# Kernel tuning notes

Measured on AMD Instinct MI355X. Metric: run time of the kernel, lower is better.

## Reference

```python
import jax, jax.numpy as jnp
import numpy as np

D_MODEL = 256
NUM_HEADS = 4
HEAD_DIM = D_MODEL // NUM_HEADS


def setup_inputs() -> dict:
    key = jax.random.key(0)
    ks = jax.random.split(key, 16)
    B, N, M, C = 2, 256, 256, D_MODEL
    inp = {
        'q_tokens': jax.random.normal(ks[0], (B, N, C), jnp.float32),
        'k_tokens': jax.random.normal(ks[1], (B, M, C), jnp.float32),
        'v_tokens': jax.random.normal(ks[2], (B, M, C), jnp.float32),
        'qk_embeds': jax.random.normal(ks[3], (B, N, M, C), jnp.float32),
        'qv_embeds': jax.random.normal(ks[4], (B, N, M, C), jnp.float32),
    }
    scale = 1.0 / np.sqrt(C)
    # Linear layer params (weight used as x @ W + b)
    inp['Wq'] = jax.random.normal(ks[5], (C, C), jnp.float32) * scale
    inp['bq'] = jnp.zeros((C,), jnp.float32)
    inp['Wk'] = jax.random.normal(ks[6], (C, C), jnp.float32) * scale
    inp['bk'] = jnp.zeros((C,), jnp.float32)
    inp['Wv'] = jax.random.normal(ks[7], (C, C), jnp.float32) * scale
    inp['bv'] = jnp.zeros((C,), jnp.float32)
    inp['Wqk'] = jax.random.normal(ks[8], (C, C), jnp.float32) * scale
    inp['bqk'] = jnp.zeros((C,), jnp.float32)
    inp['Wqv'] = jax.random.normal(ks[9], (C, C), jnp.float32) * scale
    inp['bqv'] = jnp.zeros((C,), jnp.float32)
    return inp


def reference(q_tokens, k_tokens, v_tokens, qk_embeds, qv_embeds,
              Wq, bq, Wk, bk, Wv, bv, Wqk, bqk, Wqv, bqv):
    B, N, C = q_tokens.shape
    M = k_tokens.shape[1]
    H, hc = NUM_HEADS, HEAD_DIM

    # token projections -> (B, H, len, hc)
    q = (q_tokens @ Wq + bq).reshape(B, N, H, hc).transpose(0, 2, 1, 3)
    k = (k_tokens @ Wk + bk).reshape(B, M, H, hc).transpose(0, 2, 1, 3)
    v = (v_tokens @ Wv + bv).reshape(B, M, H, hc).transpose(0, 2, 1, 3)

    # pair-embedding projections -> (B, N, M, H, hc)
    qk = (qk_embeds @ Wqk + bqk).reshape(B, N, M, H, hc)
    qv = (qv_embeds @ Wqv + bqv).reshape(B, N, M, H, hc)

    # scores: q . (k + qk)  == q.k + q.qk
    scores = jnp.einsum('bhnc,bhmc->bhnm', q, k)
    scores = scores + jnp.einsum('bhnc,bnmhc->bhnm', q, qk)
    scores = scores / np.sqrt(hc).astype(np.float32)

    attn = jax.nn.softmax(scores, axis=-1)  # (B, H, N, M)

    # output: attn @ (v + qv) == attn@v + attn.qv
    hidden = jnp.einsum('bhnm,bhmc->bhnc', attn, v)
    hidden = hidden + jnp.einsum('bhnm,bnmhc->bhnc', attn, qv)
    hidden = hidden.transpose(0, 2, 1, 3).reshape(B, N, C)  # (B, N, C)
    return hidden, attn
```

## Files before the change

### kernel.cpp

```cpp
#include <hip/hip_runtime.h>

#define BB 2
#define NN 256
#define CC 256

__device__ __forceinline__ float dot4acc(float4 e, float4 w, float s) {
    s = fmaf(e.x, w.x, s); s = fmaf(e.y, w.y, s);
    s = fmaf(e.z, w.z, s); s = fmaf(e.w, w.w, s);
    return s;
}

#define GLL(gaddr, laddr)                                                     \
    __builtin_amdgcn_global_load_lds(                                         \
        (const __attribute__((address_space(1))) void*)(gaddr),               \
        (__attribute__((address_space(3))) void*)(laddr), 16, 0, 0)

#define STAGE_TILE(B, SRCBASE, TT)                                            \
    do {                                                                      \
        const float* _g = (SRCBASE) + (size_t)(TT) * 4096;                    \
        GLL(_g + (w * 2) * 256 + l * 4,     (B) + (w * 2) * 256);             \
        GLL(_g + (w * 2 + 1) * 256 + l * 4, (B) + (w * 2 + 1) * 256);         \
    } while (0)

__global__ __launch_bounds__(256) void proj_gemm(
    const float* __restrict__ q_tok, const float* __restrict__ k_tok, const float* __restrict__ v_tok,
    const float* __restrict__ Wq, const float* __restrict__ bq,
    const float* __restrict__ Wk, const float* __restrict__ bk,
    const float* __restrict__ Wv, const float* __restrict__ bv,
    float* __restrict__ out)
{
    const int row0 = blockIdx.x * 64;
    const int col0 = blockIdx.y * 64;
    const int seg  = row0 >> 9;
    const float* A    = seg == 0 ? q_tok : (seg == 1 ? k_tok : v_tok);
    const float* W    = seg == 0 ? Wq    : (seg == 1 ? Wk    : Wv);
    const float* bias = seg == 0 ? bq    : (seg == 1 ? bk    : bv);
    const int ar0 = row0 & 511;

    __shared__ float As[64][17];
    __shared__ float Bs[16][68];
    const int t  = threadIdx.x;
    const int tr = t >> 4, tc = t & 15;
    float acc[4][4] = {};

    const int sr  = t >> 2, sk4 = (t & 3) << 2;
    const int bkr = t >> 4, bj4 = (t & 15) << 2;

    for (int k0 = 0; k0 < 256; k0 += 16) {
        float4 a4 = *reinterpret_cast<const float4*>(&A[(ar0 + sr) * 256 + k0 + sk4]);
        float4 b4 = *reinterpret_cast<const float4*>(&W[(k0 + bkr) * 256 + col0 + bj4]);
        As[sr][sk4 + 0] = a4.x; As[sr][sk4 + 1] = a4.y; As[sr][sk4 + 2] = a4.z; As[sr][sk4 + 3] = a4.w;
        Bs[bkr][bj4 + 0] = b4.x; Bs[bkr][bj4 + 1] = b4.y; Bs[bkr][bj4 + 2] = b4.z; Bs[bkr][bj4 + 3] = b4.w;
        __syncthreads();
        #pragma unroll
        for (int k = 0; k < 16; ++k) {
            float a[4], bbv[4];
            #pragma unroll
            for (int i = 0; i < 4; ++i) a[i] = As[tr * 4 + i][k];
            #pragma unroll
            for (int j = 0; j < 4; ++j) bbv[j] = Bs[k][tc * 4 + j];
            #pragma unroll
            for (int i = 0; i < 4; ++i)
                #pragma unroll
                for (int j = 0; j < 4; ++j)
                    acc[i][j] = fmaf(a[i], bbv[j], acc[i][j]);
        }
        __syncthreads();
    }
    #pragma unroll
    for (int i = 0; i < 4; ++i) {
        const int r = row0 + tr * 4 + i;
        #pragma unroll
        for (int j = 0; j < 4; ++j) {
            const int cj = col0 + tc * 4 + j;
            out[r * 256 + cj] = acc[i][j] + bias[cj];
        }
    }
}

__global__ __launch_bounds__(256) void qw_gemm(
    const float* __restrict__ qp, const float* __restrict__ Wqk, float* __restrict__ qW)
{
    const int h    = blockIdx.z;
    const int row0 = blockIdx.x * 64;
    const int d0   = blockIdx.y * 64;
    __shared__ float As[64][17];
    __shared__ float Bs[16][68];
    const int t  = threadIdx.x;
    const int tr = t >> 4, tc = t & 15;
    float acc[4][4] = {};
    const int sr = t >> 2, sc4 = (t & 3) << 2;

    for (int k0 = 0; k0 < 64; k0 += 16) {
        float4 a4 = *reinterpret_cast<const float4*>(&qp[(row0 + sr) * 256 + h * 64 + k0 + sc4]);
        float4 b4 = *reinterpret_cast<const float4*>(&Wqk[(d0 + sr) * 256 + h * 64 + k0 + sc4]);
        As[sr][sc4 + 0] = a4.x; As[sr][sc4 + 1] = a4.y; As[sr][sc4 + 2] = a4.z; As[sr][sc4 + 3] = a4.w;
        Bs[sc4 + 0][sr] = b4.x; Bs[sc4 + 1][sr] = b4.y; Bs[sc4 + 2][sr] = b4.z; Bs[sc4 + 3][sr] = b4.w;
        __syncthreads();
        #pragma unroll
        for (int k = 0; k < 16; ++k) {
            float a[4], bbv[4];
            #pragma unroll
            for (int i = 0; i < 4; ++i) a[i] = As[tr * 4 + i][k];
            #pragma unroll
            for (int j = 0; j < 4; ++j) bbv[j] = Bs[k][tc * 4 + j];
            #pragma unroll
            for (int i = 0; i < 4; ++i)
                #pragma unroll
                for (int j = 0; j < 4; ++j)
                    acc[i][j] = fmaf(a[i], bbv[j], acc[i][j]);
        }
        __syncthreads();
    }
    #pragma unroll
    for (int i = 0; i < 4; ++i)
        #pragma unroll
        for (int j = 0; j < 4; ++j)
            qW[((row0 + tr * 4 + i) * 4 + h) * 256 + d0 + tc * 4 + j] = acc[i][j];
}

__global__ __launch_bounds__(256) void qk_gemm(
    const float* __restrict__ qkvp, float* __restrict__ Sqk)
{
    const int bh = blockIdx.z;
    const int b  = bh >> 2, h = bh & 3;
    const int n0 = blockIdx.x * 64;
    const int m0 = blockIdx.y * 64;
    __shared__ float As[64][17];
    __shared__ float Bs[16][68];
    const int t  = threadIdx.x;
    const int tr = t >> 4, tc = t & 15;
    float acc[4][4] = {};
    const int sr = t >> 2, sc4 = (t & 3) << 2;

    for (int k0 = 0; k0 < 64; k0 += 16) {
        float4 a4 = *reinterpret_cast<const float4*>(&qkvp[(size_t)(b * 256 + n0 + sr) * 256 + h * 64 + k0 + sc4]);
        float4 b4 = *reinterpret_cast<const float4*>(&qkvp[(size_t)(512 + b * 256 + m0 + sr) * 256 + h * 64 + k0 + sc4]);
        As[sr][sc4 + 0] = a4.x; As[sr][sc4 + 1] = a4.y; As[sr][sc4 + 2] = a4.z; As[sr][sc4 + 3] = a4.w;
        Bs[sc4 + 0][sr] = b4.x; Bs[sc4 + 1][sr] = b4.y; Bs[sc4 + 2][sr] = b4.z; Bs[sc4 + 3][sr] = b4.w;
        __syncthreads();
        #pragma unroll
        for (int k = 0; k < 16; ++k) {
            float a[4], bbv[4];
            #pragma unroll
            for (int i = 0; i < 4; ++i) a[i] = As[tr * 4 + i][k];
            #pragma unroll
            for (int j = 0; j < 4; ++j) bbv[j] = Bs[k][tc * 4 + j];
            #pragma unroll
            for (int i = 0; i < 4; ++i)
                #pragma unroll
                for (int j = 0; j < 4; ++j)
                    acc[i][j] = fmaf(a[i], bbv[j], acc[i][j]);
        }
        __syncthreads();
    }
    #pragma unroll
    for (int i = 0; i < 4; ++i)
        #pragma unroll
        for (int j = 0; j < 4; ++j)
            Sqk[(size_t)((b * 4 + h) * 256 + n0 + tr * 4 + i) * 256 + m0 + tc * 4 + j] = acc[i][j];
}

__global__ __launch_bounds__(512, 4) void mega6(
    const float* __restrict__ qk_emb, const float* __restrict__ qv_emb,
    const float* __restrict__ qkvp, const float* __restrict__ qW,
    const float* __restrict__ Sqk, const float* __restrict__ Wqv,
    const float* __restrict__ bqv,
    float* __restrict__ attn_out, float* __restrict__ hidden)
{
    const int bn = blockIdx.x;
    const int b  = bn >> 8, n = bn & 255;
    const int t  = threadIdx.x;
    const int w  = t >> 6, l = t & 63;

    __shared__ __align__(16) float buf0[4096];
    __shared__ __align__(16) float buf1[4096];
    __shared__ __align__(16) float qWs[1024];
    __shared__ __align__(16) float SqkL[1024];
    __shared__ __align__(16) float Ssc[1024];
    __shared__ __align__(16) float attn_s[1024];
    __shared__ __align__(16) float Ap[4096];
    __shared__ __align__(16) float pr[2][256];
    __shared__ float mxs[8][4], sums[8][4];

    const float* qkb = qk_emb + (size_t)bn * 65536;
    const float* qvb = qv_emb + (size_t)bn * 65536;

    STAGE_TILE(buf0, qkb, 0);
    {
        const int i2 = t * 2;
        *reinterpret_cast<float2*>(&qWs[i2]) =
            *reinterpret_cast<const float2*>(&qW[(size_t)bn * 1024 + i2]);
        const int h = i2 >> 8, m = i2 & 255;
        *reinterpret_cast<float2*>(&SqkL[i2]) =
            *reinterpret_cast<const float2*>(&Sqk[(size_t)((b * 4 + h) * 256 + n) * 256 + m]);
    }
    __syncthreads();

    const int rl  = l >> 5;
    const int sub = l & 31;
    const int lq  = sub & 15;
    const int hp  = sub >> 4;
    const int rloc = w * 2 + rl;
    const int h0 = hp * 2, h1 = hp * 2 + 1;

    float4 qr0[4], qr1[4];
    #pragma unroll
    for (int c = 0; c < 4; ++c) {
        qr0[c] = *reinterpret_cast<const float4*>(&qWs[h0 * 256 + c * 64 + lq * 4]);
        qr1[c] = *reinterpret_cast<const float4*>(&qWs[h1 * 256 + c * 64 + lq * 4]);
    }

    for (int tt = 0; tt < 16; ++tt) {
        float* cur = (tt & 1) ? buf1 : buf0;
        float* nxt = (tt & 1) ? buf0 : buf1;
        if (tt < 15) STAGE_TILE(nxt, qkb, tt + 1);

        const float* er = cur + rloc * 256 + lq * 4;
        const float4 e0 = *reinterpret_cast<const float4*>(er);
        const float4 e1 = *reinterpret_cast<const float4*>(er + 64);
        const float4 e2 = *reinterpret_cast<const float4*>(er + 128);
        const float4 e3 = *reinterpret_cast<const float4*>(er + 192);
        float s0 = 0.f, s1 = 0.f;
        s0 = dot4acc(e0, qr0[0], s0); s0 = dot4acc(e1, qr0[1], s0);
        s0 = dot4acc(e2, qr0[2], s0); s0 = dot4acc(e3, qr0[3], s0);
        s1 = dot4acc(e0, qr1[0], s1); s1 = dot4acc(e1, qr1[1], s1);
        s1 = dot4acc(e2, qr1[2], s1); s1 = dot4acc(e3, qr1[3], s1);
        s0 += __shfl_xor(s0, 1); s1 += __shfl_xor(s1, 1);
        s0 += __shfl_xor(s0, 2); s1 += __shfl_xor(s1, 2);
        s0 += __shfl_xor(s0, 4); s1 += __shfl_xor(s1, 4);
        s0 += __shfl_xor(s0, 8); s1 += __shfl_xor(s1, 8);
        if ((l & 15) == 0) {
            const int m = tt * 16 + rloc;
            Ssc[h0 * 256 + m] = s0;
            Ssc[h1 * 256 + m] = s1;
        }
        __syncthreads();
    }

    STAGE_TILE(buf0, qvb, 0);

    const int li = l & 31;
    {
        float mxw[4], smw[4];
        #pragma unroll
        for (int h = 0; h < 4; ++h) {
            const float sc = (Ssc[h * 256 + w * 32 + li] + SqkL[h * 256 + w * 32 + li]) * 0.125f;
            float mx = sc;
            #pragma unroll
            for (int mask = 16; mask >= 1; mask >>= 1) mx = fmaxf(mx, __shfl_xor(mx, mask));
            const float e = __expf(sc - mx);
            if (l < 32) attn_s[h * 256 + w * 32 + li] = e;
            float sm = e;
            #pragma unroll
            for (int mask = 16; mask >= 1; mask >>= 1) sm += __shfl_xor(sm, mask);
            mxw[h] = mx; smw[h] = sm;
        }
        if (l == 0) {
            #pragma unroll
            for (int h = 0; h < 4; ++h) { mxs[w][h] = mxw[h]; sums[w][h] = smw[h]; }
        }
    }
    __syncthreads();

    {
        float mgv[4], invv[4];
        #pragma unroll
        for (int h = 0; h < 4; ++h) {
            float mg = mxs[0][h];
            #pragma unroll
            for (int ww = 1; ww < 8; ++ww) mg = fmaxf(mg, mxs[ww][h]);
            float sg = 0.f;
            #pragma unroll
            for (int ww = 0; ww < 8; ++ww) sg += sums[ww][h] * __expf(mxs[ww][h] - mg);
            mgv[h] = mg; invv[h] = 1.f / sg;
        }
        const int h2 = t >> 7, j = t & 127;
        float* ao = attn_out + (size_t)((b * 4 + h2) * 256 + n) * 256;
        #pragma unroll
        for (int rep = 0; rep < 2; ++rep) {
            const int jj = j + rep * 128;
            const float s = __expf(mxs[jj >> 5][h2] - mgv[h2]) * invv[h2];
            const float a = attn_s[h2 * 256 + jj] * s;
            attn_s[h2 * 256 + jj] = a;
            ao[jj] = a;
        }
    }
    __syncthreads();

    float4 acc[4];
    #pragma unroll
    for (int hh = 0; hh < 4; ++hh) acc[hh] = make_float4(0.f, 0.f, 0.f, 0.f);

    for (int tt = 0; tt < 16; ++tt) {
        float* cur = (tt & 1) ? buf1 : buf0;
        float* nxt = (tt & 1) ? buf0 : buf1;
        if (tt < 15) STAGE_TILE(nxt, qvb, tt + 1);

        const int m0 = tt * 16 + w * 2;
        const float4 e0 = *reinterpret_cast<const float4*>(&cur[(w * 2) * 256 + l * 4]);
        const float4 e1 = *reinterpret_cast<const float4*>(&cur[(w * 2 + 1) * 256 + l * 4]);
        #pragma unroll
        for (int hh = 0; hh < 4; ++hh) {
            const float a0 = attn_s[hh * 256 + m0];
            const float a1 = attn_s[hh * 256 + m0 + 1];
            acc[hh].x = fmaf(a0, e0.x, acc[hh].x); acc[hh].y = fmaf(a0, e0.y, acc[hh].y);
            acc[hh].z = fmaf(a0, e0.z, acc[hh].z); acc[hh].w = fmaf(a0, e0.w, acc[hh].w);
            acc[hh].x = fmaf(a1, e1.x, acc[hh].x); acc[hh].y = fmaf(a1, e1.y, acc[hh].y);
            acc[hh].z = fmaf(a1, e1.z, acc[hh].z); acc[hh].w = fmaf(a1, e1.w, acc[hh].w);
        }
        __syncthreads();
    }

    if (w < 4) {
        #pragma unroll
        for (int hh = 0; hh < 4; ++hh)
            *reinterpret_cast<float4*>(&Ap[(w * 4 + hh) * 256 + l * 4]) = acc[hh];
    }
    __syncthreads();
    if (w >= 4) {
        #pragma unroll
        for (int hh = 0; hh < 4; ++hh) {
            float4* p = reinterpret_cast<float4*>(&Ap[((w - 4) * 4 + hh) * 256 + l * 4]);
            float4 o = *p;
            o.x += acc[hh].x; o.y += acc[hh].y; o.z += acc[hh].z; o.w += acc[hh].w;
            *p = o;
        }
    }
    __syncthreads();
    #pragma unroll
    for (int i = 0; i < 2; ++i) {
        const int idx = t + i * 512;
        const int hh = idx >> 8, d = idx & 255;
        Ap[hh * 256 + d] = Ap[hh * 256 + d] + Ap[(4 + hh) * 256 + d]
                         + Ap[(8 + hh) * 256 + d] + Ap[(12 + hh) * 256 + d];
    }

    {
        float* stg = buf0;
        const int c = t & 255, half = t >> 8, hc = c >> 6;
        const int fr0 = t >> 6, fc0 = (t & 63) * 4;
        const int fr1 = fr0 + 8;
        const float* vbase = qkvp + (size_t)(1024 + b * 256) * 256;
        float4 ra = *reinterpret_cast<const float4*>(&vbase[(size_t)fr0 * 256 + fc0]);
        float4 rb = *reinterpret_cast<const float4*>(&vbase[(size_t)fr1 * 256 + fc0]);
        float hv = 0.f;
        for (int mt = 0; mt < 16; ++mt) {
            __syncthreads();
            *reinterpret_cast<float4*>(&stg[fr0 * 256 + fc0]) = ra;
            *reinterpret_cast<float4*>(&stg[fr1 * 256 + fc0]) = rb;
            if (mt < 15) {
                ra = *reinterpret_cast<const float4*>(&vbase[(size_t)((mt + 1) * 16 + fr0) * 256 + fc0]);
                rb = *reinterpret_cast<const float4*>(&vbase[(size_t)((mt + 1) * 16 + fr1) * 256 + fc0]);
            } else {
                ra = *reinterpret_cast<const float4*>(&Wqv[(size_t)fr0 * 256 + fc0]);
                rb = *reinterpret_cast<const float4*>(&Wqv[(size_t)fr1 * 256 + fc0]);
            }
            __syncthreads();
            #pragma unroll
            for (int r = 0; r < 8; ++r)
                hv = fmaf(attn_s[hc * 256 + mt * 16 + half * 8 + r], stg[(half * 8 + r) * 256 + c], hv);
        }
        for (int dt = 0; dt < 16; ++dt) {
            __syncthreads();
            *reinterpret_cast<float4*>(&stg[fr0 * 256 + fc0]) = ra;
            *reinterpret_cast<float4*>(&stg[fr1 * 256 + fc0]) = rb;
            if (dt < 15) {
                ra = *reinterpret_cast<const float4*>(&Wqv[(size_t)((dt + 1) * 16 + fr0) * 256 + fc0]);
                rb = *reinterpret_cast<const float4*>(&Wqv[(size_t)((dt + 1) * 16 + fr1) * 256 + fc0]);
            }
            __syncthreads();
            #pragma unroll
            for (int r = 0; r < 8; ++r)
                hv = fmaf(Ap[hc * 256 + dt * 16 + half * 8 + r], stg[(half * 8 + r) * 256 + c], hv);
        }
        pr[half][c] = hv;
    }
    __syncthreads();
    if (t < 256)
        hidden[(size_t)bn * 256 + t] = pr[0][t] + pr[1][t] + bqv[t];
}

extern "C" void kernel_launch(void* const* d_in, const int* in_sizes, int n_in,
                              void* d_out, int out_size, void* d_ws, size_t ws_size,
                              hipStream_t stream) {
    (void)in_sizes; (void)n_in; (void)out_size; (void)ws_size;
    const float* q_tok  = (const float*)d_in[0];
    const float* k_tok  = (const float*)d_in[1];
    const float* v_tok  = (const float*)d_in[2];
    const float* qk_emb = (const float*)d_in[3];
    const float* qv_emb = (const float*)d_in[4];
    const float* Wq  = (const float*)d_in[5];   const float* bq  = (const float*)d_in[6];
    const float* Wk  = (const float*)d_in[7];   const float* bk  = (const float*)d_in[8];
    const float* Wv  = (const float*)d_in[9];   const float* bv  = (const float*)d_in[10];
    const float* Wqk = (const float*)d_in[11];
    const float* Wqv = (const float*)d_in[13];  const float* bqv = (const float*)d_in[14];

    float* ws   = (float*)d_ws;
    float* qkvp = ws;
    float* qW   = ws + 393216;
    float* Sqk  = ws + 917504;

    float* hidden = (float*)d_out;
    float* attn   = (float*)d_out + BB * NN * CC;

    proj_gemm<<<dim3(24, 4),   256, 0, stream>>>(q_tok, k_tok, v_tok, Wq, bq, Wk, bk, Wv, bv, qkvp);
    qw_gemm  <<<dim3(8, 4, 4), 256, 0, stream>>>(qkvp, Wqk, qW);
    qk_gemm  <<<dim3(4, 4, 8), 256, 0, stream>>>(qkvp, Sqk);
    mega6    <<<512,           512, 0, stream>>>(qk_emb, qv_emb, qkvp, qW, Sqk, Wqv, bqv, attn, hidden);
}
```

Before: 93.41 us.

## Split pair-embedding streaming across M-quarters with split-softmax merge and output GEMM

```diff
diff --git a/kernel.cpp b/kernel.cpp
--- a/kernel.cpp
+++ b/kernel.cpp
@@ -15,9 +15,9 @@
         (const __attribute__((address_space(1))) void*)(gaddr),               \
         (__attribute__((address_space(3))) void*)(laddr), 16, 0, 0)
 
-#define STAGE_TILE(B, SRCBASE, TT)                                            \
+#define STAGE8(B, SRC, TT)                                                    \
     do {                                                                      \
-        const float* _g = (SRCBASE) + (size_t)(TT) * 4096;                    \
+        const float* _g = (SRC) + (size_t)(TT) * 2048;                        \
         GLL(_g + (w * 2) * 256 + l * 4,     (B) + (w * 2) * 256);             \
         GLL(_g + (w * 2 + 1) * 256 + l * 4, (B) + (w * 2 + 1) * 256);         \
     } while (0)
@@ -161,48 +161,39 @@
             Sqk[(size_t)((b * 4 + h) * 256 + n0 + tr * 4 + i) * 256 + m0 + tc * 4 + j] = acc[i][j];
 }
 
-__global__ __launch_bounds__(512, 4) void mega6(
+__global__ __launch_bounds__(256, 6) void stream_kernel(
     const float* __restrict__ qk_emb, const float* __restrict__ qv_emb,
-    const float* __restrict__ qkvp, const float* __restrict__ qW,
-    const float* __restrict__ Sqk, const float* __restrict__ Wqv,
-    const float* __restrict__ bqv,
-    float* __restrict__ attn_out, float* __restrict__ hidden)
+    const float* __restrict__ qW, const float* __restrict__ Sqk,
+    float* __restrict__ Sg, float* __restrict__ stats, float* __restrict__ Aq)
 {
     const int bn = blockIdx.x;
+    const int q  = blockIdx.y;
     const int b  = bn >> 8, n = bn & 255;
     const int t  = threadIdx.x;
     const int w  = t >> 6, l = t & 63;
 
-    __shared__ __align__(16) float buf0[4096];
-    __shared__ __align__(16) float buf1[4096];
+    __shared__ __align__(16) float buf0[2048];
+    __shared__ __align__(16) float buf1[2048];
     __shared__ __align__(16) float qWs[1024];
-    __shared__ __align__(16) float SqkL[1024];
-    __shared__ __align__(16) float Ssc[1024];
-    __shared__ __align__(16) float attn_s[1024];
-    __shared__ __align__(16) float Ap[4096];
-    __shared__ __align__(16) float pr[2][256];
-    __shared__ float mxs[8][4], sums[8][4];
-
-    const float* qkb = qk_emb + (size_t)bn * 65536;
-    const float* qvb = qv_emb + (size_t)bn * 65536;
-
-    STAGE_TILE(buf0, qkb, 0);
+    __shared__ __align__(16) float SqkL[256];
+    __shared__ __align__(16) float Ssc[256];
+    __shared__ __align__(16) float attn_e[256];
+
+    const float* qkb = qk_emb + (size_t)bn * 65536 + (size_t)q * 16384;
+    const float* qvb = qv_emb + (size_t)bn * 65536 + (size_t)q * 16384;
+
+    STAGE8(buf0, qkb, 0);
+    *reinterpret_cast<float4*>(&qWs[t * 4]) =
+        *reinterpret_cast<const float4*>(&qW[(size_t)bn * 1024 + t * 4]);
     {
-        const int i2 = t * 2;
-        *reinterpret_cast<float2*>(&qWs[i2]) =
-            *reinterpret_cast<const float2*>(&qW[(size_t)bn * 1024 + i2]);
-        const int h = i2 >> 8, m = i2 & 255;
-        *reinterpret_cast<float2*>(&SqkL[i2]) =
-            *reinterpret_cast<const float2*>(&Sqk[(size_t)((b * 4 + h) * 256 + n) * 256 + m]);
+        const int h = t >> 6, mi = t & 63;
+        SqkL[t] = Sqk[(size_t)((b * 4 + h) * 256 + n) * 256 + q * 64 + mi];
     }
     __syncthreads();
 
-    const int rl  = l >> 5;
-    const int sub = l & 31;
-    const int lq  = sub & 15;
-    const int hp  = sub >> 4;
-    const int rloc = w * 2 + rl;
-    const int h0 = hp * 2, h1 = hp * 2 + 1;
+    const int lq = l & 15, lr = l >> 4;
+    const int rloc = (w >> 1) * 4 + lr;
+    const int h0 = (w & 1) * 2, h1 = h0 + 1;
 
     float4 qr0[4], qr1[4];
     #pragma unroll
@@ -211,10 +202,10 @@
         qr1[c] = *reinterpret_cast<const float4*>(&qWs[h1 * 256 + c * 64 + lq * 4]);
     }
 
-    for (int tt = 0; tt < 16; ++tt) {
+    for (int tt = 0; tt < 8; ++tt) {
         float* cur = (tt & 1) ? buf1 : buf0;
         float* nxt = (tt & 1) ? buf0 : buf1;
-        if (tt < 15) STAGE_TILE(nxt, qkb, tt + 1);
+        if (tt < 7) STAGE8(nxt, qkb, tt + 1);
 
         const float* er = cur + rloc * 256 + lq * 4;
         const float4 e0 = *reinterpret_cast<const float4*>(er);
@@ -230,98 +221,70 @@
         s0 += __shfl_xor(s0, 2); s1 += __shfl_xor(s1, 2);
         s0 += __shfl_xor(s0, 4); s1 += __shfl_xor(s1, 4);
         s0 += __shfl_xor(s0, 8); s1 += __shfl_xor(s1, 8);
-        if ((l & 15) == 0) {
-            const int m = tt * 16 + rloc;
-            Ssc[h0 * 256 + m] = s0;
-            Ssc[h1 * 256 + m] = s1;
-        }
-        __syncthreads();
-    }
-
-    STAGE_TILE(buf0, qvb, 0);
-
-    const int li = l & 31;
+        if (lq == 0) {
+            const int m = tt * 8 + rloc;
+            Ssc[h0 * 64 + m] = s0;
+            Ssc[h1 * 64 + m] = s1;
+        }
+        __syncthreads();
+    }
+
+    STAGE8(buf0, qvb, 0);
+
     {
-        float mxw[4], smw[4];
-        #pragma unroll
-        for (int h = 0; h < 4; ++h) {
-            const float sc = (Ssc[h * 256 + w * 32 + li] + SqkL[h * 256 + w * 32 + li]) * 0.125f;
-            float mx = sc;
-            #pragma unroll
-            for (int mask = 16; mask >= 1; mask >>= 1) mx = fmaxf(mx, __shfl_xor(mx, mask));
-            const float e = __expf(sc - mx);
-            if (l < 32) attn_s[h * 256 + w * 32 + li] = e;
-            float sm = e;
-            #pragma unroll
-            for (int mask = 16; mask >= 1; mask >>= 1) sm += __shfl_xor(sm, mask);
-            mxw[h] = mx; smw[h] = sm;
-        }
+        const float sc = (Ssc[w * 64 + l] + SqkL[w * 64 + l]) * 0.125f;
+        float mx = sc;
+        #pragma unroll
+        for (int mask = 32; mask >= 1; mask >>= 1) mx = fmaxf(mx, __shfl_xor(mx, mask));
+        const float e = __expf(sc - mx);
+        attn_e[w * 64 + l] = e;
+        float sm = e;
+        #pragma unroll
+        for (int mask = 32; mask >= 1; mask >>= 1) sm += __shfl_xor(sm, mask);
+        Sg[(size_t)((b * 4 + w) * 256 + n) * 256 + q * 64 + l] = sc;
         if (l == 0) {
-            #pragma unroll
-            for (int h = 0; h < 4; ++h) { mxs[w][h] = mxw[h]; sums[w][h] = smw[h]; }
+            const int si = ((bn * 4 + q) * 4 + w) * 2;
+            stats[si] = mx;
+            stats[si + 1] = sm;
         }
     }
     __syncthreads();
 
-    {
-        float mgv[4], invv[4];
-        #pragma unroll
-        for (int h = 0; h < 4; ++h) {
-            float mg = mxs[0][h];
-            #pragma unroll
-            for (int ww = 1; ww < 8; ++ww) mg = fmaxf(mg, mxs[ww][h]);
-            float sg = 0.f;
-            #pragma unroll
-            for (int ww = 0; ww < 8; ++ww) sg += sums[ww][h] * __expf(mxs[ww][h] - mg);
-            mgv[h] = mg; invv[h] = 1.f / sg;
-        }
-        const int h2 = t >> 7, j = t & 127;
-        float* ao = attn_out + (size_t)((b * 4 + h2) * 256 + n) * 256;
-        #pragma unroll
-        for (int rep = 0; rep < 2; ++rep) {
-            const int jj = j + rep * 128;
-            const float s = __expf(mxs[jj >> 5][h2] - mgv[h2]) * invv[h2];
-            const float a = attn_s[h2 * 256 + jj] * s;
-            attn_s[h2 * 256 + jj] = a;
-            ao[jj] = a;
-        }
-    }
-    __syncthreads();
-
     float4 acc[4];
     #pragma unroll
     for (int hh = 0; hh < 4; ++hh) acc[hh] = make_float4(0.f, 0.f, 0.f, 0.f);
 
-    for (int tt = 0; tt < 16; ++tt) {
+    for (int tt = 0; tt < 8; ++tt) {
         float* cur = (tt & 1) ? buf1 : buf0;
         float* nxt = (tt & 1) ? buf0 : buf1;
-        if (tt < 15) STAGE_TILE(nxt, qvb, tt + 1);
-
-        const int m0 = tt * 16 + w * 2;
-        const float4 e0 = *reinterpret_cast<const float4*>(&cur[(w * 2) * 256 + l * 4]);
-        const float4 e1 = *reinterpret_cast<const float4*>(&cur[(w * 2 + 1) * 256 + l * 4]);
+        if (tt < 7) STAGE8(nxt, qvb, tt + 1);
+
+        const float4 f0 = *reinterpret_cast<const float4*>(&cur[w * 256 + l * 4]);
+        const float4 f1 = *reinterpret_cast<const float4*>(&cur[(w + 4) * 256 + l * 4]);
+        const int m0 = tt * 8 + w, m1 = tt * 8 + w + 4;
         #pragma unroll
         for (int hh = 0; hh < 4; ++hh) {
-            const float a0 = attn_s[hh * 256 + m0];
-            const float a1 = attn_s[hh * 256 + m0 + 1];
-            acc[hh].x = fmaf(a0, e0.x, acc[hh].x); acc[hh].y = fmaf(a0, e0.y, acc[hh].y);
-            acc[hh].z = fmaf(a0, e0.z, acc[hh].z); acc[hh].w = fmaf(a0, e0.w, acc[hh].w);
-            acc[hh].x = fmaf(a1, e1.x, acc[hh].x); acc[hh].y = fmaf(a1, e1.y, acc[hh].y);
-            acc[hh].z = fmaf(a1, e1.z, acc[hh].z); acc[hh].w = fmaf(a1, e1.w, acc[hh].w);
-        }
-        __syncthreads();
-    }
-
-    if (w < 4) {
+            const float a0 = attn_e[hh * 64 + m0];
+            const float a1 = attn_e[hh * 64 + m1];
+            acc[hh].x = fmaf(a0, f0.x, acc[hh].x); acc[hh].y = fmaf(a0, f0.y, acc[hh].y);
+            acc[hh].z = fmaf(a0, f0.z, acc[hh].z); acc[hh].w = fmaf(a0, f0.w, acc[hh].w);
+            acc[hh].x = fmaf(a1, f1.x, acc[hh].x); acc[hh].y = fmaf(a1, f1.y, acc[hh].y);
+            acc[hh].z = fmaf(a1, f1.z, acc[hh].z); acc[hh].w = fmaf(a1, f1.w, acc[hh].w);
+        }
+        __syncthreads();
+    }
+
+    float* Ap = buf0;
+    if (w < 2) {
         #pragma unroll
         for (int hh = 0; hh < 4; ++hh)
             *reinterpret_cast<float4*>(&Ap[(w * 4 + hh) * 256 + l * 4]) = acc[hh];
     }
     __syncthreads();
-    if (w >= 4) {
+    if (w >= 2) {
         #pragma unroll
         for (int hh = 0; hh < 4; ++hh) {
-            float4* p = reinterpret_cast<float4*>(&Ap[((w - 4) * 4 + hh) * 256 + l * 4]);
+            float4* p = reinterpret_cast<float4*>(&Ap[((w - 2) * 4 + hh) * 256 + l * 4]);
             float4 o = *p;
             o.x += acc[hh].x; o.y += acc[hh].y; o.z += acc[hh].z; o.w += acc[hh].w;
             *p = o;
@@ -329,56 +292,126 @@
     }
     __syncthreads();
     #pragma unroll
-    for (int i = 0; i < 2; ++i) {
-        const int idx = t + i * 512;
+    for (int i = 0; i < 4; ++i) {
+        const int idx = t + i * 256;
         const int hh = idx >> 8, d = idx & 255;
-        Ap[hh * 256 + d] = Ap[hh * 256 + d] + Ap[(4 + hh) * 256 + d]
-                         + Ap[(8 + hh) * 256 + d] + Ap[(12 + hh) * 256 + d];
-    }
-
-    {
-        float* stg = buf0;
-        const int c = t & 255, half = t >> 8, hc = c >> 6;
-        const int fr0 = t >> 6, fc0 = (t & 63) * 4;
-        const int fr1 = fr0 + 8;
-        const float* vbase = qkvp + (size_t)(1024 + b * 256) * 256;
-        float4 ra = *reinterpret_cast<const float4*>(&vbase[(size_t)fr0 * 256 + fc0]);
-        float4 rb = *reinterpret_cast<const float4*>(&vbase[(size_t)fr1 * 256 + fc0]);
-        float hv = 0.f;
-        for (int mt = 0; mt < 16; ++mt) {
-            __syncthreads();
-            *reinterpret_cast<float4*>(&stg[fr0 * 256 + fc0]) = ra;
-            *reinterpret_cast<float4*>(&stg[fr1 * 256 + fc0]) = rb;
-            if (mt < 15) {
-                ra = *reinterpret_cast<const float4*>(&vbase[(size_t)((mt + 1) * 16 + fr0) * 256 + fc0]);
-                rb = *reinterpret_cast<const float4*>(&vbase[(size_t)((mt + 1) * 16 + fr1) * 256 + fc0]);
-            } else {
-                ra = *reinterpret_cast<const float4*>(&Wqv[(size_t)fr0 * 256 + fc0]);
-                rb = *reinterpret_cast<const float4*>(&Wqv[(size_t)fr1 * 256 + fc0]);
-            }
-            __syncthreads();
-            #pragma unroll
-            for (int r = 0; r < 8; ++r)
-                hv = fmaf(attn_s[hc * 256 + mt * 16 + half * 8 + r], stg[(half * 8 + r) * 256 + c], hv);
-        }
-        for (int dt = 0; dt < 16; ++dt) {
-            __syncthreads();
-            *reinterpret_cast<float4*>(&stg[fr0 * 256 + fc0]) = ra;
-            *reinterpret_cast<float4*>(&stg[fr1 * 256 + fc0]) = rb;
-            if (dt < 15) {
-                ra = *reinterpret_cast<const float4*>(&Wqv[(size_t)((dt + 1) * 16 + fr0) * 256 + fc0]);
-                rb = *reinterpret_cast<const float4*>(&Wqv[(size_t)((dt + 1) * 16 + fr1) * 256 + fc0]);
-            }
-            __syncthreads();
-            #pragma unroll
-            for (int r = 0; r < 8; ++r)
-                hv = fmaf(Ap[hc * 256 + dt * 16 + half * 8 + r], stg[(half * 8 + r) * 256 + c], hv);
-        }
-        pr[half][c] = hv;
-    }
-    __syncthreads();
-    if (t < 256)
-        hidden[(size_t)bn * 256 + t] = pr[0][t] + pr[1][t] + bqv[t];
+        Aq[((size_t)(bn * 4 + q) * 4 + hh) * 256 + d] = Ap[hh * 256 + d] + Ap[(4 + hh) * 256 + d];
+    }
+}
+
+__global__ __launch_bounds__(256) void merge_kernel(
+    const float* __restrict__ Sg, const float* __restrict__ stats,
+    const float* __restrict__ Aq, float* __restrict__ attn_out,
+    float* __restrict__ Afull)
+{
+    const int bn = blockIdx.x;
+    const int b = bn >> 8, n = bn & 255;
+    const int t = threadIdx.x;
+    const int h = t >> 6, mi = t & 63;
+
+    float mx[4], sm[4];
+    #pragma unroll
+    for (int qq = 0; qq < 4; ++qq) {
+        const int si = ((bn * 4 + qq) * 4 + h) * 2;
+        mx[qq] = stats[si];
+        sm[qq] = stats[si + 1];
+    }
+    float mg = fmaxf(fmaxf(mx[0], mx[1]), fmaxf(mx[2], mx[3]));
+    float sg = 0.f;
+    #pragma unroll
+    for (int qq = 0; qq < 4; ++qq) sg += sm[qq] * __expf(mx[qq] - mg);
+    const float inv = 1.f / sg;
+
+    const size_t rowbase = (size_t)((b * 4 + h) * 256 + n) * 256;
+    #pragma unroll
+    for (int qq = 0; qq < 4; ++qq) {
+        const int m = qq * 64 + mi;
+        attn_out[rowbase + m] = __expf(Sg[rowbase + m] - mg) * inv;
+    }
+
+    float4 af = make_float4(0.f, 0.f, 0.f, 0.f);
+    #pragma unroll
+    for (int qq = 0; qq < 4; ++qq) {
+        const float scl = __expf(mx[qq] - mg) * inv;
+        const float4 v = *reinterpret_cast<const float4*>(
+            &Aq[((size_t)(bn * 4 + qq) * 4 + h) * 256 + mi * 4]);
+        af.x = fmaf(v.x, scl, af.x); af.y = fmaf(v.y, scl, af.y);
+        af.z = fmaf(v.z, scl, af.z); af.w = fmaf(v.w, scl, af.w);
+    }
+    *reinterpret_cast<float4*>(&Afull[(size_t)bn * 1024 + h * 256 + mi * 4]) = af;
+}
+
+__global__ __launch_bounds__(256) void out_gemm(
+    const float* __restrict__ qkvp, const float* __restrict__ attn,
+    const float* __restrict__ Afull, const float* __restrict__ Wqv,
+    const float* __restrict__ bqv, float* __restrict__ hidden)
+{
+    const int h  = blockIdx.y;
+    const int r0 = blockIdx.x * 64;
+    const int b  = r0 >> 8;
+    __shared__ float As[64][17];
+    __shared__ float Bs[16][68];
+    const int t  = threadIdx.x;
+    const int tr = t >> 4, tc = t & 15;
+    const int sr = t >> 2, sk4 = (t & 3) << 2;
+    const int bkr = t >> 4, bj4 = (t & 15) << 2;
+    float acc[4][4] = {};
+
+    for (int k0 = 0; k0 < 256; k0 += 16) {
+        float4 a4 = *reinterpret_cast<const float4*>(
+            &attn[(size_t)((b * 4 + h) * 256 + ((r0 + sr) & 255)) * 256 + k0 + sk4]);
+        float4 b4 = *reinterpret_cast<const float4*>(
+            &qkvp[(size_t)(1024 + b * 256 + k0 + bkr) * 256 + h * 64 + bj4]);
+        As[sr][sk4 + 0] = a4.x; As[sr][sk4 + 1] = a4.y; As[sr][sk4 + 2] = a4.z; As[sr][sk4 + 3] = a4.w;
+        Bs[bkr][bj4 + 0] = b4.x; Bs[bkr][bj4 + 1] = b4.y; Bs[bkr][bj4 + 2] = b4.z; Bs[bkr][bj4 + 3] = b4.w;
+        __syncthreads();
+        #pragma unroll
+        for (int k = 0; k < 16; ++k) {
+            float a[4], bbv[4];
+            #pragma unroll
+            for (int i = 0; i < 4; ++i) a[i] = As[tr * 4 + i][k];
+            #pragma unroll
+            for (int j = 0; j < 4; ++j) bbv[j] = Bs[k][tc * 4 + j];
+            #pragma unroll
+            for (int i = 0; i < 4; ++i)
+                #pragma unroll
+                for (int j = 0; j < 4; ++j)
+                    acc[i][j] = fmaf(a[i], bbv[j], acc[i][j]);
+        }
+        __syncthreads();
+    }
+    for (int k0 = 0; k0 < 256; k0 += 16) {
+        float4 a4 = *reinterpret_cast<const float4*>(
+            &Afull[(size_t)(r0 + sr) * 1024 + h * 256 + k0 + sk4]);
+        float4 b4 = *reinterpret_cast<const float4*>(
+            &Wqv[(size_t)(k0 + bkr) * 256 + h * 64 + bj4]);
+        As[sr][sk4 + 0] = a4.x; As[sr][sk4 + 1] = a4.y; As[sr][sk4 + 2] = a4.z; As[sr][sk4 + 3] = a4.w;
+        Bs[bkr][bj4 + 0] = b4.x; Bs[bkr][bj4 + 1] = b4.y; Bs[bkr][bj4 + 2] = b4.z; Bs[bkr][bj4 + 3] = b4.w;
+        __syncthreads();
+        #pragma unroll
+        for (int k = 0; k < 16; ++k) {
+            float a[4], bbv[4];
+            #pragma unroll
+            for (int i = 0; i < 4; ++i) a[i] = As[tr * 4 + i][k];
+            #pragma unroll
+            for (int j = 0; j < 4; ++j) bbv[j] = Bs[k][tc * 4 + j];
+            #pragma unroll
+            for (int i = 0; i < 4; ++i)
+                #pragma unroll
+                for (int j = 0; j < 4; ++j)
+                    acc[i][j] = fmaf(a[i], bbv[j], acc[i][j]);
+        }
+        __syncthreads();
+    }
+    #pragma unroll
+    for (int i = 0; i < 4; ++i) {
+        const int r = r0 + tr * 4 + i;
+        #pragma unroll
+        for (int j = 0; j < 4; ++j) {
+            const int cj = h * 64 + tc * 4 + j;
+            hidden[(size_t)r * 256 + cj] = acc[i][j] + bqv[cj];
+        }
+    }
 }
 
 extern "C" void kernel_launch(void* const* d_in, const int* in_sizes, int n_in,
@@ -396,16 +429,22 @@
     const float* Wqk = (const float*)d_in[11];
     const float* Wqv = (const float*)d_in[13];  const float* bqv = (const float*)d_in[14];
 
-    float* ws   = (float*)d_ws;
-    float* qkvp = ws;
-    float* qW   = ws + 393216;
-    float* Sqk  = ws + 917504;
+    float* ws    = (float*)d_ws;
+    float* qkvp  = ws;
+    float* qW    = ws + 393216;
+    float* Sqk   = ws + 917504;
+    float* Sg    = ws + 1441792;
+    float* stats = ws + 1966080;
+    float* Aq    = ws + 1982464;
+    float* Afull = ws + 4079616;
 
     float* hidden = (float*)d_out;
     float* attn   = (float*)d_out + BB * NN * CC;
 
-    proj_gemm<<<dim3(24, 4),   256, 0, stream>>>(q_tok, k_tok, v_tok, Wq, bq, Wk, bk, Wv, bv, qkvp);
-    qw_gemm  <<<dim3(8, 4, 4), 256, 0, stream>>>(qkvp, Wqk, qW);
-    qk_gemm  <<<dim3(4, 4, 8), 256, 0, stream>>>(qkvp, Sqk);
-    mega6    <<<512,           512, 0, stream>>>(qk_emb, qv_emb, qkvp, qW, Sqk, Wqv, bqv, attn, hidden);
-}
+    proj_gemm    <<<dim3(24, 4),   256, 0, stream>>>(q_tok, k_tok, v_tok, Wq, bq, Wk, bk, Wv, bv, qkvp);
+    qw_gemm      <<<dim3(8, 4, 4), 256, 0, stream>>>(qkvp, Wqk, qW);
+    qk_gemm      <<<dim3(4, 4, 8), 256, 0, stream>>>(qkvp, Sqk);
+    stream_kernel<<<dim3(512, 4),  256, 0, stream>>>(qk_emb, qv_emb, qW, Sqk, Sg, stats, Aq);
+    merge_kernel <<<512,           256, 0, stream>>>(Sg, stats, Aq, attn, Afull);
+    out_gemm     <<<dim3(8, 4),    256, 0, stream>>>(qkvp, attn, Afull, Wqv, bqv, hidden);
+}
```

After: 126.7 us. 35.6% more time.
